# Optimization experiments

Hardware: AMD Instinct MI355X
Metric: run time of the kernel (lower is better)

## Reference

```python
import jax, jax.numpy as jnp
import numpy as np

BATCH = 8192
IN_FEATURES = 1024
OUT_FEATURES = 1024
GRID_SIZE = 5
SPLINE_ORDER = 3
GRID_MIN, GRID_MAX = -1.0, 1.0
NUM_BASES = GRID_SIZE + SPLINE_ORDER  # 8
GRID_LEN = GRID_SIZE + 2 * SPLINE_ORDER + 1  # 12


def setup_inputs() -> dict:
    key = jax.random.key(0)
    k1, k2, k3 = jax.random.split(key, 3)
    x = jax.random.normal(k1, (BATCH, IN_FEATURES), dtype=jnp.float32)
    base_weight = jax.random.normal(k2, (OUT_FEATURES, IN_FEATURES), dtype=jnp.float32) * 0.1
    spline_weight = jax.random.normal(k3, (OUT_FEATURES, IN_FEATURES, NUM_BASES), dtype=jnp.float32) * 0.1
    grid = jnp.linspace(GRID_MIN, GRID_MAX, GRID_LEN, dtype=jnp.float32)  # buffer, not learned
    return {"x": x, "base_weight": base_weight, "spline_weight": spline_weight, "grid": grid}


def _bspline_basis(xc, grid, order):
    """Iterative Cox-de Boor DP, vectorized over all features and basis indices.
    xc: [B, F] clamped inputs; grid: [G] uniform knots (all denominators > 0).
    Returns [B, F, G - order - 1] = [B, F, NUM_BASES]."""
    G = grid.shape[0]
    xe = xc[..., None]  # [B, F, 1]
    # k = 0: indicator of knot interval, matches (x >= grid[i]) & (x < grid[i+1])
    B = ((xe >= grid[:-1]) & (xe < grid[1:])).astype(xc.dtype)  # [B, F, G-1]
    for k in range(1, order + 1):
        left = (xe - grid[: G - k - 1]) / (grid[k : G - 1] - grid[: G - k - 1]) * B[..., :-1]
        right = (grid[k + 1 : G] - xe) / (grid[k + 1 : G] - grid[1 : G - k]) * B[..., 1:]
        B = left + right  # [B, F, G-1-k]
    return B


def reference(x, base_weight, spline_weight, grid):
    # base path: SiLU activation then linear
    base_output = jax.nn.silu(x) @ base_weight.T  # [B, out]
    # spline path: B-spline basis per feature, weighted sum over (in, basis)
    x_clamped = jnp.clip(x, GRID_MIN * 0.99, GRID_MAX * 0.99)
    basis = _bspline_basis(x_clamped, grid, SPLINE_ORDER)  # [B, in, NUM_BASES]
    spline_output = jnp.einsum("bin,oin->bo", basis, spline_weight)
    return base_output + spline_output
```

## Files before the change

### kernel.cpp

```cpp
#include <hip/hip_runtime.h>
#include <stdint.h>

typedef _Float16 f16;
typedef __attribute__((ext_vector_type(8))) _Float16 f16x8;
typedef __attribute__((ext_vector_type(4))) float f32x4;

#define BATCH 8192
#define INF   1024
#define OUTF  1024
#define KTOT  9216
#define NT    72

__device__ __forceinline__ void gload16(const void* g, void* l) {
  __builtin_amdgcn_global_load_lds(
      (const __attribute__((address_space(1))) uint32_t*)g,
      (__attribute__((address_space(3))) uint32_t*)l, 16, 0, 0);
}

__global__ __launch_bounds__(256) void convert_w_kernel(
    const float* __restrict__ bw, const float* __restrict__ sw,
    f16* __restrict__ Wb)
{
  int idx = blockIdx.x * 256 + threadIdx.x;
  int o = idx / 1152;
  int r = idx - o * 1152;
  int k8 = r * 8;
  const float* src = (k8 < INF) ? (bw + (size_t)o * INF + k8)
                                : (sw + (size_t)o * (INF * 8) + (k8 - INF));
  float4 v0 = *(const float4*)src;
  float4 v1 = *(const float4*)(src + 4);
  f16x8 ov;
  ov[0] = (f16)v0.x; ov[1] = (f16)v0.y; ov[2] = (f16)v0.z; ov[3] = (f16)v0.w;
  ov[4] = (f16)v1.x; ov[5] = (f16)v1.y; ov[6] = (f16)v1.z; ov[7] = (f16)v1.w;
  *(f16x8*)(Wb + (size_t)o * KTOT + k8) = ov;
}

__global__ __launch_bounds__(256) void prep_a_kernel(
    const float* __restrict__ x, const float* __restrict__ grid,
    f16* __restrict__ Abuf)
{
  int q = blockIdx.x * 256 + threadIdx.x;
  int b = q >> 8;
  int i0 = (q & 255) << 2;
  float4 xv = *(const float4*)(x + ((size_t)b << 10) + i0);
  float xa[4] = {xv.x, xv.y, xv.z, xv.w};

  float g[12];
#pragma unroll
  for (int j = 0; j < 12; ++j) g[j] = grid[j];
  float H  = g[1] - g[0];
  float r1 = 1.0f / H;
  float r2 = 0.5f * r1;
  float r3 = (1.0f / 3.0f) * r1;

  f16 sil[4];
  f16x8 bas[4];
#pragma unroll
  for (int e = 0; e < 4; ++e) {
    float v = xa[e];
    sil[e] = (f16)(v / (1.0f + __expf(-v)));
    float xe = fminf(fmaxf(v, -0.99f), 0.99f);
    float Bv[11];
#pragma unroll
    for (int j = 0; j < 11; ++j) Bv[j] = (xe >= g[j] && xe < g[j + 1]) ? 1.0f : 0.0f;
#pragma unroll
    for (int j = 0; j < 10; ++j) Bv[j] = (xe - g[j]) * r1 * Bv[j] + (g[j + 2] - xe) * r1 * Bv[j + 1];
#pragma unroll
    for (int j = 0; j < 9; ++j)  Bv[j] = (xe - g[j]) * r2 * Bv[j] + (g[j + 3] - xe) * r2 * Bv[j + 1];
#pragma unroll
    for (int j = 0; j < 8; ++j)  Bv[j] = (xe - g[j]) * r3 * Bv[j] + (g[j + 4] - xe) * r3 * Bv[j + 1];
#pragma unroll
    for (int n = 0; n < 8; ++n) bas[e][n] = (f16)Bv[n];
  }
  f16* row = Abuf + (size_t)b * KTOT;
  *(uint64_t*)(row + i0) = *(const uint64_t*)sil;
  f16* bp = row + INF + (size_t)i0 * 8;
#pragma unroll
  for (int e = 0; e < 4; ++e) *(f16x8*)(bp + e * 8) = bas[e];
}

#define LDA(base, m, s) (*(const f16x8*)((base) + ((wr*128 + (m)*16 + la) * 64 + ((((s)*4 + lb) ^ lasw) * 8))))
#define LDB(base, n, s) (*(const f16x8*)((base) + ((wcn*64 + (n)*16 + la) * 64 + ((((s)*4 + lb) ^ lasw) * 8))))

#define MFMA1(m, n, s) acc[m][n] = __builtin_amdgcn_mfma_f32_16x16x32_f16(af[m][s], bf[n][s], acc[m][n], 0, 0, 0)
#define MFMA_PHASE(m0) do { \
  MFMA1(m0,0,0);   MFMA1(m0,1,0);   MFMA1(m0,2,0);   MFMA1(m0,3,0); \
  MFMA1(m0+1,0,0); MFMA1(m0+1,1,0); MFMA1(m0+1,2,0); MFMA1(m0+1,3,0); \
  MFMA1(m0,0,1);   MFMA1(m0,1,1);   MFMA1(m0,2,1);   MFMA1(m0,3,1); \
  MFMA1(m0+1,0,1); MFMA1(m0+1,1,1); MFMA1(m0+1,2,1); MFMA1(m0+1,3,1); \
} while (0)

#define LGKM0 do { asm volatile("s_waitcnt lgkmcnt(0)" ::: "memory"); \
                   __builtin_amdgcn_sched_barrier(0); } while (0)
#define SBAR  __builtin_amdgcn_s_barrier()
#define SCHED0 __builtin_amdgcn_sched_barrier(0)

template <bool ATOMIC>
__global__ __launch_bounds__(512, 2) void kan_gemm_kernel(
    const f16* __restrict__ A, const f16* __restrict__ W,
    float* __restrict__ C, float* __restrict__ P1)
{
  __shared__ __align__(16) f16 lsA[2 * 256 * 64];
  __shared__ __align__(16) f16 lsB[2 * 256 * 64];

  const size_t K = KTOT;
  int bid = blockIdx.x;
  int wg  = (bid & 7) * 32 + (bid >> 3);
  int tm  = wg & 31;
  int gg  = wg >> 5;
  int tn  = gg >> 1;
  int split = gg & 1;
  size_t kbase = (size_t)split * (NT * 64);

  int tid = threadIdx.x;
  int w = tid >> 6, l = tid & 63;
  int wr = w >> 2, wcn = w & 3;
  int la = l & 15, lb = l >> 4, lasw = la & 7;

  int rh = tid >> 3;
  int sc = (tid & 7) ^ (rh & 7);
  const f16* aSrc0 = A + (size_t)(tm * 256 + rh) * K + kbase + sc * 8;
  const f16* bSrc0 = W + (size_t)(tn * 256 + rh) * K + kbase + sc * 8;

  auto stage = [&](int h) {
    if (h >= 4 * NT) return;
    int tile = h >> 2, ty = h & 3, half = ty & 1;
    size_t koff = (size_t)tile * 64;
    if (ty < 2) {
      const f16* s = aSrc0 + (size_t)half * 128 * K + koff;
      f16* d = lsA + (tile & 1) * 16384 + half * 8192 + w * 512;
      gload16(s, d);
      gload16(s + 64 * K, d + 4096);
    } else {
      const f16* s = bSrc0 + (size_t)half * 128 * K + koff;
      f16* d = lsB + (tile & 1) * 16384 + half * 8192 + w * 512;
      gload16(s, d);
      gload16(s + 64 * K, d + 4096);
    }
  };

  f16x8 af[8][2], bf[4][2];
  f32x4 acc[8][4] = {};

  stage(2); stage(3); stage(0); stage(1); stage(6); stage(7);
  asm volatile("s_waitcnt vmcnt(4)" ::: "memory");
  SBAR; SCHED0;
  {
    const f16* bA = lsA; const f16* bB = lsB;
#pragma unroll
    for (int n = 0; n < 4; ++n) { bf[n][0] = LDB(bB, n, 0); bf[n][1] = LDB(bB, n, 1); }
    af[0][0] = LDA(bA, 0, 0); af[0][1] = LDA(bA, 0, 1);
    af[1][0] = LDA(bA, 1, 0); af[1][1] = LDA(bA, 1, 1);
  }

  for (int t = 0; t < NT; ++t) {
    const f16* bA  = lsA + (t & 1) * 16384;
    const f16* bB  = lsB + (t & 1) * 16384;
    const f16* bA1 = lsA + ((t + 1) & 1) * 16384;
    const f16* bB1 = lsB + ((t + 1) & 1) * 16384;
    int h1 = 4 * (t + 1), h2 = 4 * (t + 2);

    stage(h1 + 0); stage(h1 + 1);
    SCHED0; SBAR; LGKM0;
    __builtin_amdgcn_s_setprio(1);
    MFMA_PHASE(0);
    __builtin_amdgcn_s_setprio(0);
    af[2][0] = LDA(bA, 2, 0); af[2][1] = LDA(bA, 2, 1);
    af[3][0] = LDA(bA, 3, 0); af[3][1] = LDA(bA, 3, 1);
    SCHED0; SBAR;

    stage(h2 + 2);
    SCHED0; SBAR; LGKM0;
    __builtin_amdgcn_s_setprio(1);
    MFMA_PHASE(2);
    __builtin_amdgcn_s_setprio(0);
    af[4][0] = LDA(bA, 4, 0); af[4][1] = LDA(bA, 4, 1);
    af[5][0] = LDA(bA, 5, 0); af[5][1] = LDA(bA, 5, 1);
    SCHED0; SBAR;

    stage(h2 + 3);
    SCHED0; SBAR; LGKM0;
    __builtin_amdgcn_s_setprio(1);
    MFMA_PHASE(4);
    __builtin_amdgcn_s_setprio(0);
    af[6][0] = LDA(bA, 6, 0); af[6][1] = LDA(bA, 6, 1);
    af[7][0] = LDA(bA, 7, 0); af[7][1] = LDA(bA, 7, 1);
    SCHED0; SBAR;

    if (t < NT - 2)       asm volatile("s_waitcnt vmcnt(4)" ::: "memory");
    else if (t == NT - 2) asm volatile("s_waitcnt vmcnt(0)" ::: "memory");
    SCHED0; SBAR; LGKM0;
    __builtin_amdgcn_s_setprio(1);
    MFMA_PHASE(6);
    __builtin_amdgcn_s_setprio(0);
    if (t < NT - 1) {
#pragma unroll
      for (int n = 0; n < 4; ++n) { bf[n][0] = LDB(bB1, n, 0); bf[n][1] = LDB(bB1, n, 1); }
      af[0][0] = LDA(bA1, 0, 0); af[0][1] = LDA(bA1, 0, 1);
      af[1][0] = LDA(bA1, 1, 0); af[1][1] = LDA(bA1, 1, 1);
    }
    SCHED0; SBAR;
  }

  int rowBase = tm * 256 + wr * 128 + lb * 4;
  int colBase = tn * 256 + wcn * 64 + la;
  float* dst = ATOMIC ? C : (split ? P1 : C);
#pragma unroll
  for (int m = 0; m < 8; ++m)
#pragma unroll
    for (int n = 0; n < 4; ++n) {
      int col = colBase + n * 16;
#pragma unroll
      for (int j = 0; j < 4; ++j) {
        int row = rowBase + m * 16 + j;
        if (ATOMIC) atomicAdd(&C[(size_t)row * OUTF + col], acc[m][n][j]);
        else        dst[(size_t)row * OUTF + col] = acc[m][n][j];
      }
    }
}

__global__ __launch_bounds__(256) void reduce_kernel(
    float* __restrict__ out, const float* __restrict__ p)
{
  size_t i = ((size_t)blockIdx.x * 256 + threadIdx.x) * 4;
  f32x4 a = *(f32x4*)(out + i);
  f32x4 b = *(const f32x4*)(p + i);
  a += b;
  *(f32x4*)(out + i) = a;
}

extern "C" void kernel_launch(void* const* d_in, const int* in_sizes, int n_in,
                              void* d_out, int out_size, void* d_ws, size_t ws_size,
                              hipStream_t stream)
{
  const float* x  = (const float*)d_in[0];
  const float* bw = (const float*)d_in[1];
  const float* sw = (const float*)d_in[2];
  const float* gr = (const float*)d_in[3];
  float* out = (float*)d_out;

  f16* Wb = (f16*)d_ws;
  size_t wBytes = (size_t)OUTF * KTOT * sizeof(f16);
  f16* Abuf = (f16*)((char*)d_ws + wBytes);
  size_t aBytes = (size_t)BATCH * KTOT * sizeof(f16);
  size_t oBytes = (size_t)BATCH * OUTF * sizeof(float);

  convert_w_kernel<<<(OUTF * (KTOT / 8)) / 256, 256, 0, stream>>>(bw, sw, Wb);
  prep_a_kernel<<<(BATCH * INF / 4) / 256, 256, 0, stream>>>(x, gr, Abuf);

  if (ws_size >= wBytes + aBytes + oBytes) {
    float* P1 = (float*)((char*)d_ws + wBytes + aBytes);
    kan_gemm_kernel<false><<<256, 512, 0, stream>>>(Abuf, Wb, out, P1);
    reduce_kernel<<<(int)(oBytes / sizeof(float) / 4 / 256), 256, 0, stream>>>(out, P1);
  } else {
    hipMemsetAsync(d_out, 0, oBytes, stream);
    kan_gemm_kernel<true><<<256, 512, 0, stream>>>(Abuf, Wb, out, nullptr);
  }
}
```

Baseline: 218.6 us.

## Fuse prep kernels and interleave LDS fragment loads between MFMA halves

The weight-conversion and activation-prep kernels are merged into one launch, with the block index selecting which job a block does. This removes a launch boundary and lets the two memory-bound jobs share the device. In the GEMM main loop, each MFMA phase is split into two halves with the next A/B fragment LDS reads placed between them. Most explicit sched_barriers are also dropped, so LDS latency can hide under matrix work. The risk is that the compiler reorders instructions less favourably or register pressure rises without the scheduling fences.

```diff
diff --git a/kernel.cpp b/kernel.cpp
--- a/kernel.cpp
+++ b/kernel.cpp
@@ -10,6 +10,7 @@
 #define OUTF  1024
 #define KTOT  9216
 #define NT    72
+#define CONV_BLOCKS 4608
 
 __device__ __forceinline__ void gload16(const void* g, void* l) {
   __builtin_amdgcn_global_load_lds(
@@ -17,29 +18,29 @@
       (__attribute__((address_space(3))) uint32_t*)l, 16, 0, 0);
 }
 
-__global__ __launch_bounds__(256) void convert_w_kernel(
+__global__ __launch_bounds__(256) void fused_prep_kernel(
     const float* __restrict__ bw, const float* __restrict__ sw,
-    f16* __restrict__ Wb)
-{
-  int idx = blockIdx.x * 256 + threadIdx.x;
-  int o = idx / 1152;
-  int r = idx - o * 1152;
-  int k8 = r * 8;
-  const float* src = (k8 < INF) ? (bw + (size_t)o * INF + k8)
-                                : (sw + (size_t)o * (INF * 8) + (k8 - INF));
-  float4 v0 = *(const float4*)src;
-  float4 v1 = *(const float4*)(src + 4);
-  f16x8 ov;
-  ov[0] = (f16)v0.x; ov[1] = (f16)v0.y; ov[2] = (f16)v0.z; ov[3] = (f16)v0.w;
-  ov[4] = (f16)v1.x; ov[5] = (f16)v1.y; ov[6] = (f16)v1.z; ov[7] = (f16)v1.w;
-  *(f16x8*)(Wb + (size_t)o * KTOT + k8) = ov;
-}
-
-__global__ __launch_bounds__(256) void prep_a_kernel(
     const float* __restrict__ x, const float* __restrict__ grid,
-    f16* __restrict__ Abuf)
-{
-  int q = blockIdx.x * 256 + threadIdx.x;
+    f16* __restrict__ Wb, f16* __restrict__ Abuf)
+{
+  int blk = blockIdx.x;
+  if (blk < CONV_BLOCKS) {
+    int idx = blk * 256 + threadIdx.x;
+    int o = idx / 1152;
+    int r = idx - o * 1152;
+    int k8 = r * 8;
+    const float* src = (k8 < INF) ? (bw + (size_t)o * INF + k8)
+                                  : (sw + (size_t)o * (INF * 8) + (k8 - INF));
+    float4 v0 = *(const float4*)src;
+    float4 v1 = *(const float4*)(src + 4);
+    f16x8 ov;
+    ov[0] = (f16)v0.x; ov[1] = (f16)v0.y; ov[2] = (f16)v0.z; ov[3] = (f16)v0.w;
+    ov[4] = (f16)v1.x; ov[5] = (f16)v1.y; ov[6] = (f16)v1.z; ov[7] = (f16)v1.w;
+    *(f16x8*)(Wb + (size_t)o * KTOT + k8) = ov;
+    return;
+  }
+
+  int q = (blk - CONV_BLOCKS) * 256 + threadIdx.x;
   int b = q >> 8;
   int i0 = (q & 255) << 2;
   float4 xv = *(const float4*)(x + ((size_t)b << 10) + i0);
@@ -83,17 +84,16 @@
 #define LDB(base, n, s) (*(const f16x8*)((base) + ((wcn*64 + (n)*16 + la) * 64 + ((((s)*4 + lb) ^ lasw) * 8))))
 
 #define MFMA1(m, n, s) acc[m][n] = __builtin_amdgcn_mfma_f32_16x16x32_f16(af[m][s], bf[n][s], acc[m][n], 0, 0, 0)
-#define MFMA_PHASE(m0) do { \
+#define MFMA_S0(m0) do { \
   MFMA1(m0,0,0);   MFMA1(m0,1,0);   MFMA1(m0,2,0);   MFMA1(m0,3,0); \
-  MFMA1(m0+1,0,0); MFMA1(m0+1,1,0); MFMA1(m0+1,2,0); MFMA1(m0+1,3,0); \
+  MFMA1(m0+1,0,0); MFMA1(m0+1,1,0); MFMA1(m0+1,2,0); MFMA1(m0+1,3,0); } while (0)
+#define MFMA_S1(m0) do { \
   MFMA1(m0,0,1);   MFMA1(m0,1,1);   MFMA1(m0,2,1);   MFMA1(m0,3,1); \
-  MFMA1(m0+1,0,1); MFMA1(m0+1,1,1); MFMA1(m0+1,2,1); MFMA1(m0+1,3,1); \
-} while (0)
+  MFMA1(m0+1,0,1); MFMA1(m0+1,1,1); MFMA1(m0+1,2,1); MFMA1(m0+1,3,1); } while (0)
 
 #define LGKM0 do { asm volatile("s_waitcnt lgkmcnt(0)" ::: "memory"); \
                    __builtin_amdgcn_sched_barrier(0); } while (0)
 #define SBAR  __builtin_amdgcn_s_barrier()
-#define SCHED0 __builtin_amdgcn_sched_barrier(0)
 
 template <bool ATOMIC>
 __global__ __launch_bounds__(512, 2) void kan_gemm_kernel(
@@ -144,7 +144,7 @@
 
   stage(2); stage(3); stage(0); stage(1); stage(6); stage(7);
   asm volatile("s_waitcnt vmcnt(4)" ::: "memory");
-  SBAR; SCHED0;
+  SBAR;
   {
     const f16* bA = lsA; const f16* bB = lsB;
 #pragma unroll
@@ -161,45 +161,51 @@
     int h1 = 4 * (t + 1), h2 = 4 * (t + 2);
 
     stage(h1 + 0); stage(h1 + 1);
-    SCHED0; SBAR; LGKM0;
-    __builtin_amdgcn_s_setprio(1);
-    MFMA_PHASE(0);
-    __builtin_amdgcn_s_setprio(0);
+    SBAR; LGKM0;
+    __builtin_amdgcn_s_setprio(1);
+    MFMA_S0(0);
     af[2][0] = LDA(bA, 2, 0); af[2][1] = LDA(bA, 2, 1);
     af[3][0] = LDA(bA, 3, 0); af[3][1] = LDA(bA, 3, 1);
-    SCHED0; SBAR;
+    MFMA_S1(0);
+    __builtin_amdgcn_s_setprio(0);
+    SBAR;
 
     stage(h2 + 2);
-    SCHED0; SBAR; LGKM0;
-    __builtin_amdgcn_s_setprio(1);
-    MFMA_PHASE(2);
-    __builtin_amdgcn_s_setprio(0);
+    SBAR; LGKM0;
+    __builtin_amdgcn_s_setprio(1);
+    MFMA_S0(2);
     af[4][0] = LDA(bA, 4, 0); af[4][1] = LDA(bA, 4, 1);
     af[5][0] = LDA(bA, 5, 0); af[5][1] = LDA(bA, 5, 1);
-    SCHED0; SBAR;
+    MFMA_S1(2);
+    __builtin_amdgcn_s_setprio(0);
+    SBAR;
 
     stage(h2 + 3);
-    SCHED0; SBAR; LGKM0;
-    __builtin_amdgcn_s_setprio(1);
-    MFMA_PHASE(4);
-    __builtin_amdgcn_s_setprio(0);
+    SBAR; LGKM0;
+    __builtin_amdgcn_s_setprio(1);
+    MFMA_S0(4);
     af[6][0] = LDA(bA, 6, 0); af[6][1] = LDA(bA, 6, 1);
     af[7][0] = LDA(bA, 7, 0); af[7][1] = LDA(bA, 7, 1);
-    SCHED0; SBAR;
+    MFMA_S1(4);
+    __builtin_amdgcn_s_setprio(0);
+    SBAR;
 
     if (t < NT - 2)       asm volatile("s_waitcnt vmcnt(4)" ::: "memory");
     else if (t == NT - 2) asm volatile("s_waitcnt vmcnt(0)" ::: "memory");
-    SCHED0; SBAR; LGKM0;
-    __builtin_amdgcn_s_setprio(1);
-    MFMA_PHASE(6);
-    __builtin_amdgcn_s_setprio(0);
+    SBAR; LGKM0;
+    __builtin_amdgcn_s_setprio(1);
+    MFMA_S0(6);
     if (t < NT - 1) {
-#pragma unroll
-      for (int n = 0; n < 4; ++n) { bf[n][0] = LDB(bB1, n, 0); bf[n][1] = LDB(bB1, n, 1); }
       af[0][0] = LDA(bA1, 0, 0); af[0][1] = LDA(bA1, 0, 1);
       af[1][0] = LDA(bA1, 1, 0); af[1][1] = LDA(bA1, 1, 1);
     }
-    SCHED0; SBAR;
+    MFMA_S1(6);
+    __builtin_amdgcn_s_setprio(0);
+    if (t < NT - 1) {
+#pragma unroll
+      for (int n = 0; n < 4; ++n) { bf[n][0] = LDB(bB1, n, 0); bf[n][1] = LDB(bB1, n, 1); }
+    }
+    SBAR;
   }
 
   int rowBase = tm * 256 + wr * 128 + lb * 4;
@@ -245,8 +251,9 @@
   size_t aBytes = (size_t)BATCH * KTOT * sizeof(f16);
   size_t oBytes = (size_t)BATCH * OUTF * sizeof(float);
 
-  convert_w_kernel<<<(OUTF * (KTOT / 8)) / 256, 256, 0, stream>>>(bw, sw, Wb);
-  prep_a_kernel<<<(BATCH * INF / 4) / 256, 256, 0, stream>>>(x, gr, Abuf);
+  int prepBlocks = (BATCH * INF / 4) / 256;
+  fused_prep_kernel<<<CONV_BLOCKS + prepBlocks, 256, 0, stream>>>(
+      bw, sw, x, gr, Wb, Abuf);
 
   if (ws_size >= wBytes + aBytes + oBytes) {
     float* P1 = (float*)((char*)d_ws + wBytes + aBytes);
```

After: 219.1 us. Within noise of the previous version (+0.2%).
